# Performance work log

Measured on AMD Instinct MI355X. Metric: run time of the kernel, lower is better.

Reference implementation:

```python
import jax, jax.numpy as jnp
import numpy as np
from jax import lax

B, H, W, C = 8, 64, 64, 256  # H must equal W (einsum contraction requires it)
CQ = C // 4


def conv2d(x, w, b, dilation=1):
    # x: NHWC, w: HWIO (TF Conv2D layout), padding 'same'
    y = lax.conv_general_dilated(
        x, w, window_strides=(1, 1), padding='SAME',
        rhs_dilation=(dilation, dilation),
        dimension_numbers=('NHWC', 'HWIO', 'NHWC'))
    return y + b


def setup_inputs() -> dict:
    key = jax.random.key(0)
    ks = jax.random.split(key, 16)
    s = 0.05
    inp = {
        'x':   jax.random.normal(ks[0], (B, H, W, C), jnp.float32),
        'wq':  jax.random.normal(ks[1], (1, 1, C, CQ), jnp.float32) * s,
        'bq':  jnp.zeros((CQ,), jnp.float32),
        'wq1': jax.random.normal(ks[2], (3, 3, C, CQ), jnp.float32) * s,
        'bq1': jnp.zeros((CQ,), jnp.float32),
        'wq2': jax.random.normal(ks[3], (3, 3, C, CQ), jnp.float32) * s,
        'bq2': jnp.zeros((CQ,), jnp.float32),
        'wq3': jax.random.normal(ks[4], (3, 3, C, CQ), jnp.float32) * s,
        'bq3': jnp.zeros((CQ,), jnp.float32),
        'wq4': jax.random.normal(ks[5], (1, 1, C, C), jnp.float32) * s,
        'bq4': jnp.zeros((C,), jnp.float32),
        'wk':  jax.random.normal(ks[6], (3, 3, C, C), jnp.float32) * s,
        'bk':  jnp.zeros((C,), jnp.float32),
        'wv':  jax.random.normal(ks[7], (1, 1, C, C), jnp.float32) * s,
        'bv':  jnp.zeros((C,), jnp.float32),
        'gamma': jax.random.normal(ks[8], (1,), jnp.float32) * 0.1,
    }
    return inp


def reference(x, wq, bq, wq1, bq1, wq2, bq2, wq3, bq3, wq4, bq4,
              wk, bk, wv, bv, gamma):
    # multi-scale query branch: 1x1, 3x3, 3x3 dil=3, 3x3 dil=6 -> concat -> 1x1
    q = jnp.concatenate([
        conv2d(x, wq, bq, 1),
        conv2d(x, wq1, bq1, 1),
        conv2d(x, wq2, bq2, 3),
        conv2d(x, wq3, bq3, 6),
    ], axis=-1)
    q = conv2d(q, wq4, bq4, 1)                 # (B,H,W,C)
    # key conv applied twice with the SAME weights (as in the original code)
    k = conv2d(conv2d(x, wk, bk, 1), wk, bk, 1)  # (B,H,W,C)
    v = conv2d(x, wv, bv, 1)                    # (B,H,W,C)

    qT = jnp.transpose(q, (0, 2, 1, 3))         # (B,W,H,C)
    # per-channel spatial contraction; requires H == W
    energy = jnp.einsum('bijc,bkjc->bikc', k, qT)   # (B,H,W,C)
    attention = jax.nn.softmax(energy, axis=-1)     # softmax over CHANNEL axis
    attnT = jnp.transpose(attention, (0, 2, 1, 3))  # (B,W,H,C)
    out = jnp.einsum('bijc,bkjc->bikc', attnT, v)   # (B,W,H,C)
    return gamma * out + x
```

## Files before the change

kernel.cpp:

```cpp
#include <hip/hip_runtime.h>

typedef short  short8 __attribute__((ext_vector_type(8)));
typedef short  sv4    __attribute__((ext_vector_type(4)));
typedef __bf16 bf16x8 __attribute__((ext_vector_type(8)));
typedef float  f32x4  __attribute__((ext_vector_type(4)));

__device__ __forceinline__ float bf2f(short s) {
    unsigned u = ((unsigned)(unsigned short)s) << 16;
    return __builtin_bit_cast(float, u);
}
__device__ __forceinline__ short f2bf(float f) {
    unsigned u = __builtin_bit_cast(unsigned, f);
    u += 0x7fffu + ((u >> 16) & 1u);
    return (short)(u >> 16);
}
__device__ __forceinline__ f32x4 mfma16(short8 a, short8 b, f32x4 c) {
    return __builtin_amdgcn_mfma_f32_16x16x32_bf16(
        __builtin_bit_cast(bf16x8, a), __builtin_bit_cast(bf16x8, b), c, 0, 0, 0);
}
__device__ __forceinline__ void gl16(const short* g, short* l) {
    __builtin_amdgcn_global_load_lds(
        (const __attribute__((address_space(1))) void*)g,
        (__attribute__((address_space(3))) void*)l, 16, 0, 0);
}


__global__ __launch_bounds__(256) void detect_k(const short* x, int* flag)
{
    __shared__ int red[256];
    int t = threadIdx.x;
    int cnt = 0;
    for (int i = t; i < 4096; i += 256) {
        int e = (x[2 * i] >> 7) & 0xFF;
        cnt += (e >= 100 && e <= 140) ? 1 : 0;
    }
    red[t] = cnt; __syncthreads();
    for (int s = 128; s > 0; s >>= 1) { if (t < s) red[t] += red[t + s]; __syncthreads(); }
    if (t == 0) *flag = (red[0] < 3277) ? 1 : 0;
}

__global__ __launch_bounds__(256) void convert_x(const void* x, short* xb, const int* flagp)
{
    int f32 = *flagp;
    size_t i = ((size_t)blockIdx.x * 256 + threadIdx.x) * 8;
    short8 v;
    if (f32) {
        const float* fs = (const float*)x + i;
        f32x4 a = *(const f32x4*)fs;
        f32x4 b = *(const f32x4*)(fs + 4);
#pragma unroll
        for (int l = 0; l < 4; l++) { v[l] = f2bf(a[l]); v[4 + l] = f2bf(b[l]); }
    } else {
        v = *(const short8*)((const short*)x + i);
    }
    *(short8*)(xb + i) = v;
}

struct Ptrs {
    const void *wq, *wq1, *wq2, *wq3, *wq4, *wk, *wv;
    const void *bq, *bq1, *bq2, *bq3, *bq4, *bk, *bv, *gm;
};

__global__ __launch_bounds__(256) void convert_k(Ptrs P, short* wp, short* bb, const int* flagp)
{
    int f32 = *flagp;
    int idx = blockIdx.x * 256 + threadIdx.x;
    if (idx < 1179648) {
        const void* src; int Cout, base;
        if      (idx <   16384) { src = P.wq;  Cout =  64; base = 0; }
        else if (idx <  163840) { src = P.wq1; Cout =  64; base = 16384; }
        else if (idx <  311296) { src = P.wq2; Cout =  64; base = 163840; }
        else if (idx <  458752) { src = P.wq3; Cout =  64; base = 311296; }
        else if (idx <  524288) { src = P.wq4; Cout = 256; base = 458752; }
        else if (idx < 1114112) { src = P.wk;  Cout = 256; base = 524288; }
        else                    { src = P.wv;  Cout = 256; base = 1114112; }
        int rem = idx - base;
        int t   = rem / (Cout * 256);
        int r2  = rem - t * Cout * 256;
        int co  = r2 >> 8;
        int ci  = r2 & 255;
        int si  = (t * 256 + ci) * Cout + co;
        wp[idx] = f32 ? f2bf(((const float*)src)[si]) : ((const short*)src)[si];
    } else if (idx < 1179648 + 1280) {
        int j = idx - 1179648;
        if (j < 1025) {
            const void* src; int off;
            if      (j <   64) { src = P.bq;  off = j; }
            else if (j <  128) { src = P.bq1; off = j - 64; }
            else if (j <  192) { src = P.bq2; off = j - 128; }
            else if (j <  256) { src = P.bq3; off = j - 192; }
            else if (j <  512) { src = P.bq4; off = j - 256; }
            else if (j <  768) { src = P.bk;  off = j - 512; }
            else if (j < 1024) { src = P.bv;  off = j - 768; }
            else               { src = P.gm;  off = 0; }
            bb[j] = f32 ? f2bf(((const float*)src)[off]) : ((const short*)src)[off];
        } else if (j >= 1032) {
            bb[j] = 0;
        }
    }
}

struct C8Job {
    const short* src;
    short*       dst;
    const short* wpk;
    const short* bias;
    int outmode;
};

__global__ __launch_bounds__(512, 2) void conv8_tile(C8Job J, const short* zp)
{
    __shared__ short Sh[49152];
    int tid  = threadIdx.x;
    int wid  = tid >> 6, lane = tid & 63;
    int bid  = blockIdx.x;
    int Mtile = (bid & 7) * 32 + (bid >> 3);
    int p0 = Mtile * 128;
    int b  = p0 >> 12;
    int h0 = (p0 >> 6) & 63;

    int lrow = lane & 15, quad = lane >> 4;
    int lr8  = lane >> 3;
    int cl   = (lane & 7) ^ (lr8 & 7);
    int m_base = (wid >> 2) * 64;
    int n_base = (wid & 3) * 64;

    const short* aroot[2]; unsigned vmask[2];
#pragma unroll
    for (int jj = 0; jj < 2; jj++) {
        int m  = (jj * 8 + wid) * 8 + lr8;
        int hh = h0 + (m >> 6);
        int ww = m & 63;
        aroot[jj] = J.src + (((b * 64 + hh) * 64 + ww) * 256 + cl * 8);
        unsigned msk = 0;
#pragma unroll
        for (int t = 0; t < 9; ++t) {
            int dy = t / 3 - 1, dx = t % 3 - 1;
            bool v = ((unsigned)(hh + dy) < 64u) && ((unsigned)(ww + dx) < 64u);
            msk |= (v ? 1u : 0u) << t;
        }
        vmask[jj] = msk;
    }
    const short* wroot[4];
#pragma unroll
    for (int jj = 0; jj < 4; jj++) {
        int n = (jj * 8 + wid) * 8 + lr8;
        wroot[jj] = J.wpk + n * 256 + cl * 8;
    }

    auto STAGE = [&](int step) {
        int t = step >> 2, s4 = step & 3;
        int dy = t / 3 - 1, dx = t % 3 - 1;
        int tdel = (dy * 64 + dx) * 256 + s4 * 64;
        short* bufb = Sh + (step & 1) * 24576;
#pragma unroll
        for (int jj = 0; jj < 2; jj++) {
            const short* p = ((vmask[jj] >> t) & 1u) ? (aroot[jj] + tdel) : (zp + s4 * 64);
            gl16(p, bufb + (jj * 8 + wid) * 512);
        }
#pragma unroll
        for (int jj = 0; jj < 4; jj++)
            gl16(wroot[jj] + t * 65536 + s4 * 64, bufb + 8192 + (jj * 8 + wid) * 512);
    };

    f32x4 acc[4][4] = {};
    STAGE(0);
    for (int s = 0; s < 36; ++s) {
        if (s < 35) {
            STAGE(s + 1);
            asm volatile("s_waitcnt vmcnt(6)" ::: "memory");
        } else {
            asm volatile("s_waitcnt vmcnt(0)" ::: "memory");
        }
        __builtin_amdgcn_sched_barrier(0);
        __builtin_amdgcn_s_barrier();
        __builtin_amdgcn_sched_barrier(0);
        const short* bufb = Sh + (s & 1) * 24576;
#pragma unroll
        for (int j = 0; j < 2; j++) {
            int pc = ((j * 4 + quad) ^ (lrow & 7)) * 8;
            short8 a4[4], b4[4];
#pragma unroll
            for (int mi = 0; mi < 4; mi++)
                a4[mi] = *(const short8*)(bufb + (m_base + mi * 16 + lrow) * 64 + pc);
#pragma unroll
            for (int ni = 0; ni < 4; ni++)
                b4[ni] = *(const short8*)(bufb + 8192 + (n_base + ni * 16 + lrow) * 64 + pc);
            __builtin_amdgcn_s_setprio(1);
#pragma unroll
            for (int mi = 0; mi < 4; mi++)
#pragma unroll
                for (int ni = 0; ni < 4; ni++)
                    acc[mi][ni] = mfma16(a4[mi], b4[ni], acc[mi][ni]);
            __builtin_amdgcn_s_setprio(0);
        }
        __builtin_amdgcn_sched_barrier(0);
        __builtin_amdgcn_s_barrier();
        __builtin_amdgcn_sched_barrier(0);
    }

    int rq = quad * 4;
#pragma unroll
    for (int ni = 0; ni < 4; ni++) {
        int co = n_base + ni * 16 + lrow;
        float bv = bf2f(J.bias[co]);
        if (J.outmode == 0) {
#pragma unroll
            for (int mi = 0; mi < 4; mi++) {
                int pb = p0 + m_base + mi * 16 + rq;
#pragma unroll
                for (int r = 0; r < 4; r++)
                    J.dst[(size_t)(pb + r) * 256 + co] = f2bf(acc[mi][ni][r] + bv);
            }
        } else {
            int hw = h0 + (m_base >> 6);
            short* row = J.dst + ((size_t)(b * 256 + co) * 64 + hw) * 64;
#pragma unroll
            for (int mi = 0; mi < 4; mi++) {
                sv4 o;
#pragma unroll
                for (int r = 0; r < 4; r++) o[r] = f2bf(acc[mi][ni][r] + bv);
                *(sv4*)(row + mi * 16 + rq) = o;
            }
        }
    }
}

struct CJob {
    const short* src;
    short*       dst;
    const short* wpk;
    const short* bias;
    int Cout;
    int dil;
    int ntaps;
    int coff;
    int outmode;
};
struct CTable { CJob j[6]; int end[6]; };

template<int NA, int NB, int BOFS, int WSTEP>
__device__ __forceinline__ void conv_loop(
    const short* src, const short* wpk, int ntaps, int dil,
    const short* zp, short* Sh,
    int wave, int lr8, int cl, int h0, int b, int nt0, int srcT,
    int m_base, int n_base, int lrow, int pc0, int pc1,
    f32x4 (&acc)[4][4])
{
    const short* abase[NA];
    unsigned     vm[NA];
    const short* bbase[NB];
#pragma unroll
    for (int jj = 0; jj < NA; jj++) {
        int m  = (jj * 4 + wave) * 8 + lr8;
        int hh = srcT ? (m & 63) : (h0 + (m >> 6));
        int ww = srcT ? (h0 + (m >> 6)) : (m & 63);
        abase[jj] = src + (((b * 64 + hh) * 64 + ww) * 256 + cl * 8);
        unsigned msk = 1u;
        if (ntaps == 9) {
            msk = 0u;
#pragma unroll
            for (int t = 0; t < 9; ++t) {
                int tr = (t >= 6) ? 2 : ((t >= 3) ? 1 : 0);
                int dy = (tr - 1) * dil, dx = (t - tr * 3 - 1) * dil;
                bool v = ((unsigned)(hh + dy) < 64u) && ((unsigned)(ww + dx) < 64u);
                msk |= (v ? 1u : 0u) << t;
            }
        }
        vm[jj] = msk;
    }
#pragma unroll
    for (int jj = 0; jj < NB; jj++) {
        int n = (jj * 4 + wave) * 8 + lr8;
        bbase[jj] = wpk + (nt0 + n) * 256 + cl * 8;
    }

    int prevdel = 0;
    for (int t = 0; t < ntaps; ++t) {
        int dy = 0, dx = 0;
        if (ntaps == 9) {
            int tr = (t >= 6) ? 2 : ((t >= 3) ? 1 : 0);
            dy = (tr - 1) * dil;
            dx = (t - tr * 3 - 1) * dil;
        }
        int tdel = (dy * 64 + dx) * 256;
        int step = tdel - prevdel; prevdel = tdel;
        const short* pA[NA];
#pragma unroll
        for (int jj = 0; jj < NA; jj++) {
            abase[jj] += step;
            pA[jj] = ((vm[jj] >> t) & 1u) ? abase[jj] : zp;
        }
#pragma unroll
        for (int s4 = 0; s4 < 4; ++s4) {
#pragma unroll
            for (int jj = 0; jj < NA; jj++)
                gl16(pA[jj] + s4 * 64, Sh + (jj * 4 + wave) * 512);
#pragma unroll
            for (int jj = 0; jj < NB; jj++)
                gl16(bbase[jj] + s4 * 64, Sh + BOFS + (jj * 4 + wave) * 512);
            __syncthreads();
#pragma unroll
            for (int j = 0; j < 2; j++) {
                int pc = j ? pc1 : pc0;
                short8 a4[4], b4[4];
#pragma unroll
                for (int mi = 0; mi < 4; mi++)
                    a4[mi] = *(const short8*)(Sh + (m_base + mi * 16 + lrow) * 64 + pc);
#pragma unroll
                for (int ni = 0; ni < 4; ni++)
                    b4[ni] = *(const short8*)(Sh + BOFS + (n_base + ni * 16 + lrow) * 64 + pc);
#pragma unroll
                for (int mi = 0; mi < 4; mi++)
#pragma unroll
                    for (int ni = 0; ni < 4; ni++)
                        acc[mi][ni] = mfma16(a4[mi], b4[ni], acc[mi][ni]);
            }
            __syncthreads();
        }
#pragma unroll
        for (int jj = 0; jj < NB; jj++) bbase[jj] += WSTEP;
    }
}

__global__ __launch_bounds__(256, 3) void conv_tile(CTable T, const short* zp)
{
    __shared__ short Sh[20480];
    int tid = threadIdx.x;
    int bid = blockIdx.x;
    int ji = 0;
    while (ji < 5 && bid >= T.end[ji]) ji++;
    CJob J = T.j[ji];
    int s0  = ji ? T.end[ji - 1] : 0;
    int seg = T.end[ji] - s0;
    int lb  = bid - s0;
    int g   = (lb & 7) * (seg >> 3) + (lb >> 3);

    int big   = (J.Cout == 256);
    int BM    = big ? 128 : 256;
    int ntile = big ? (g & 1) : 0;
    int Mtile = big ? (g >> 1) : g;
    int p0 = Mtile * BM;
    int b  = p0 >> 12;
    int h0 = (p0 >> 6) & 63;
    int nt0  = ntile * 128;
    int srcT = (J.outmode == 3);

    int wave = tid >> 6, lane = tid & 63;
    int lrow = lane & 15, quad = lane >> 4;
    int m_base = big ? (wave & 1) * 64 : wave * 64;
    int n_base = big ? (wave >> 1) * 64 : 0;

    int lr8 = lane >> 3;
    int cl  = (lane & 7) ^ (lr8 & 7);

    int pc0 = ((quad     ^ (lrow & 7)) * 8);
    int pc1 = (((4 + quad) ^ (lrow & 7)) * 8);

    f32x4 acc[4][4] = {};
    if (big)
        conv_loop<4, 4, 8192, 65536>(J.src, J.wpk, J.ntaps, J.dil, zp, Sh,
                                     wave, lr8, cl, h0, b, nt0, srcT,
                                     m_base, n_base, lrow, pc0, pc1, acc);
    else
        conv_loop<8, 2, 16384, 16384>(J.src, J.wpk, J.ntaps, J.dil, zp, Sh,
                                      wave, lr8, cl, h0, b, nt0, srcT,
                                      m_base, n_base, lrow, pc0, pc1, acc);

    int rq = quad * 4;
#pragma unroll
    for (int ni = 0; ni < 4; ni++) {
        int co = nt0 + n_base + ni * 16 + lrow;
        float bv = bf2f(J.bias[co]);
        if (J.outmode == 0) {
#pragma unroll
            for (int mi = 0; mi < 4; mi++) {
                int pb = p0 + m_base + mi * 16 + rq;
#pragma unroll
                for (int r = 0; r < 4; r++)
                    J.dst[(size_t)(pb + r) * 256 + J.coff + co] = f2bf(acc[mi][ni][r] + bv);
            }
        } else {
            int hw = h0 + (m_base >> 6);
            short* row = J.dst + ((size_t)(b * 256 + co) * 64 + hw) * 64;
#pragma unroll
            for (int mi = 0; mi < 4; mi++) {
                sv4 o;
#pragma unroll
                for (int r = 0; r < 4; r++) o[r] = f2bf(acc[mi][ni][r] + bv);
                *(sv4*)(row + mi * 16 + rq) = o;
            }
        }
    }
}

__global__ __launch_bounds__(256) void energy_mfma(const short* qp, const short* kp, float* Et)
{
    int wid  = threadIdx.x >> 6;
    int lane = threadIdx.x & 63;
    int g = blockIdx.x * 4 + wid;
    int b = g >> 8, c = g & 255;
    int lrow = lane & 15;
    int q8   = (lane >> 4) << 3;
    const short* qb = qp + (size_t)(b * 256 + c) * 4096;
    const short* kb = kp + (size_t)(b * 256 + c) * 4096;

    f32x4 acc[4][4] = {};
#pragma unroll
    for (int ks = 0; ks < 2; ++ks) {
        int j0 = ks * 32 + q8;
        short8 A[4], Bv[4];
#pragma unroll
        for (int mi = 0; mi < 4; mi++)
            A[mi] = *(const short8*)(qb + (size_t)(mi * 16 + lrow) * 64 + j0);
#pragma unroll
        for (int ni = 0; ni < 4; ni++)
            Bv[ni] = *(const short8*)(kb + (size_t)(ni * 16 + lrow) * 64 + j0);
#pragma unroll
        for (int mi = 0; mi < 4; mi++)
#pragma unroll
            for (int ni = 0; ni < 4; ni++)
                acc[mi][ni] = mfma16(A[mi], Bv[ni], acc[mi][ni]);
    }
    int rq = (lane >> 4) * 4;
#pragma unroll
    for (int mi = 0; mi < 4; mi++)
#pragma unroll
        for (int r = 0; r < 4; r++) {
            int w = mi * 16 + rq + r;
            float* row = Et + ((size_t)(b * 256 + c) * 64 + w) * 64;
#pragma unroll
            for (int ni = 0; ni < 4; ni++)
                row[ni * 16 + lrow] = acc[mi][ni][r];
        }
}

__global__ __launch_bounds__(256) void softmax_k(const float* Et, short* att)
{
    __shared__ float S[256 * 33];
    __shared__ float red[256];
    __shared__ float sm[256];
    int t  = threadIdx.x;
    int b  = blockIdx.x >> 7;
    int a  = (blockIdx.x >> 1) & 63;
    int jh = blockIdx.x & 1;

    const float* row = Et + ((size_t)(b * 256 + t) * 64 + a) * 64 + jh * 32;
#pragma unroll
    for (int jj = 0; jj < 32; jj += 4) {
        f32x4 v = *(const f32x4*)(row + jj);
#pragma unroll
        for (int l = 0; l < 4; l++) S[t * 33 + jj + l] = v[l];
    }
    __syncthreads();

    int tj = t & 31, tg = t >> 5;
    float m = -1e30f;
#pragma unroll
    for (int cc = 0; cc < 32; ++cc) m = fmaxf(m, S[(tg * 32 + cc) * 33 + tj]);
    red[t] = m;
    __syncthreads();
    if (tg == 0) {
        float mm = red[tj];
#pragma unroll
        for (int gg = 1; gg < 8; ++gg) mm = fmaxf(mm, red[gg * 32 + tj]);
        red[tj] = mm;
    }
    __syncthreads();
    float M = red[tj];
    float s = 0.f;
#pragma unroll
    for (int cc = 0; cc < 32; ++cc) {
        int id = (tg * 32 + cc) * 33 + tj;
        float e = __expf(S[id] - M);
        S[id] = e; s += e;
    }
    sm[t] = s;
    __syncthreads();
    if (tg == 0) {
        float ss = sm[tj];
#pragma unroll
        for (int gg = 1; gg < 8; ++gg) ss += sm[gg * 32 + tj];
        sm[tj] = 1.0f / ss;
    }
    __syncthreads();

    short* orow = att + ((size_t)(b * 256 + t) * 64 + a) * 64 + jh * 32;
#pragma unroll
    for (int jj = 0; jj < 32; jj += 8) {
        short8 o;
#pragma unroll
        for (int l = 0; l < 8; l++) o[l] = f2bf(S[t * 33 + jj + l] * sm[jj + l]);
        *(short8*)(orow + jj) = o;
    }
}

__global__ __launch_bounds__(256) void out_mfma(const short* vp, const short* att, short* G)
{
    int wid  = threadIdx.x >> 6;
    int lane = threadIdx.x & 63;
    int g = blockIdx.x * 4 + wid;
    int b = g >> 8, c = g & 255;
    int lrow = lane & 15;
    int q8   = (lane >> 4) << 3;
    const short* vb = vp  + (size_t)(b * 256 + c) * 4096;
    const short* ab = att + (size_t)(b * 256 + c) * 4096;

    f32x4 acc[4][4] = {};
#pragma unroll
    for (int ks = 0; ks < 2; ++ks) {
        int j0 = ks * 32 + q8;
        short8 A[4], Bv[4];
#pragma unroll
        for (int mi = 0; mi < 4; mi++)
            A[mi] = *(const short8*)(vb + (size_t)(mi * 16 + lrow) * 64 + j0);
#pragma unroll
        for (int ni = 0; ni < 4; ni++)
            Bv[ni] = *(const short8*)(ab + (size_t)(ni * 16 + lrow) * 64 + j0);
#pragma unroll
        for (int mi = 0; mi < 4; mi++)
#pragma unroll
            for (int ni = 0; ni < 4; ni++)
                acc[mi][ni] = mfma16(A[mi], Bv[ni], acc[mi][ni]);
    }
    int rq = (lane >> 4) * 4;
#pragma unroll
    for (int mi = 0; mi < 4; mi++)
#pragma unroll
        for (int r = 0; r < 4; r++) {
            int d = mi * 16 + rq + r;
            short* row = G + ((size_t)(b * 256 + c) * 64 + d) * 64;
#pragma unroll
            for (int ni = 0; ni < 4; ni++)
                row[ni * 16 + lrow] = f2bf(acc[mi][ni][r]);
        }
}

__global__ __launch_bounds__(256) void final_k(const short* G, const void* x,
                                               const void* gamma, void* out, const int* flagp)
{
    int f32 = *flagp;
    int t = threadIdx.x;
    int b = blockIdx.x >> 6, r = blockIdx.x & 63;
    const short* grow = G + ((size_t)(b * 256 + t) * 64 + r) * 64;
    float gm = f32 ? ((const float*)gamma)[0] : bf2f(((const short*)gamma)[0]);
    size_t obase = ((size_t)(b * 64) * 64 + r) * 256 + t;
    if (f32) {
        const float* xs = (const float*)x;
        float* os = (float*)out;
#pragma unroll
        for (int p8 = 0; p8 < 8; p8++) {
            short8 gv = *(const short8*)(grow + p8 * 8);
#pragma unroll
            for (int l = 0; l < 8; l++) {
                size_t off = obase + (size_t)(p8 * 8 + l) * 16384;
                os[off] = gm * bf2f(gv[l]) + xs[off];
            }
        }
    } else {
        const short* xs = (const short*)x;
        short* os = (short*)out;
#pragma unroll
        for (int p8 = 0; p8 < 8; p8++) {
            short8 gv = *(const short8*)(grow + p8 * 8);
#pragma unroll
            for (int l = 0; l < 8; l++) {
                size_t off = obase + (size_t)(p8 * 8 + l) * 16384;
                os[off] = f2bf(gm * bf2f(gv[l]) + bf2f(xs[off]));
            }
        }
    }
}

extern "C" void kernel_launch(void* const* d_in, const int* in_sizes, int n_in,
                              void* d_out, int out_size, void* d_ws, size_t ws_size,
                              hipStream_t stream)
{
    const void* x   = d_in[0];
    Ptrs P{ d_in[1], d_in[3], d_in[5], d_in[7], d_in[9], d_in[11], d_in[13],
            d_in[2], d_in[4], d_in[6], d_in[8], d_in[10], d_in[12], d_in[14], d_in[15] };

    short* ws   = (short*)d_ws;
    short* qcat = ws;
    short* k1   = ws + 8388608;
    short* qp   = ws + 16777216;
    short* kp   = ws + 25165824;
    short* vp   = ws + 33554432;
    short* wp   = ws + 41943040;
    short* bb   = ws + 43122688;
    int*   flag = (int*)(ws + 43123968);
    short* xb   = qp;
    float* Et   = (float*)d_ws;
    short* att  = qp;
    short* G    = kp;
    const short* zp = bb + 1032;

    detect_k<<<1, 256, 0, stream>>>((const short*)x, flag);
    convert_x<<<4096, 256, 0, stream>>>(x, xb, flag);
    convert_k<<<4613, 256, 0, stream>>>(P, wp, bb, flag);

    C8Job A8{ xb, k1, wp + 524288, bb + 512, 0 };
    conv8_tile<<<256, 512, 0, stream>>>(A8, zp);

    CJob j1{ xb, qcat, wp + 16384,   bb + 64,  64,  1, 9, 64,  0 };
    CJob j2{ xb, qcat, wp + 163840,  bb + 128, 64,  3, 9, 128, 0 };
    CJob j3{ xb, qcat, wp + 311296,  bb + 192, 64,  6, 9, 192, 0 };
    CJob jb{ xb, vp,   wp + 1114112, bb + 768, 256, 1, 1, 0,   2 };
    CJob ja{ xb, qcat, wp + 0,       bb + 0,   64,  1, 1, 0,   0 };
    CTable TA{ { j1, j2, j3, jb, ja, ja }, { 128, 256, 384, 896, 1024, 1024 } };
    conv_tile<<<1024, 256, 0, stream>>>(TA, zp);

    C8Job B8{ k1, kp, wp + 524288, bb + 512, 2 };
    conv8_tile<<<256, 512, 0, stream>>>(B8, zp);

    CJob j5{ qcat, qp, wp + 458752, bb + 256, 256, 1, 1, 0, 3 };
    CTable TB{ { j5, j5, j5, j5, j5, j5 }, { 512, 512, 512, 512, 512, 512 } };
    conv_tile<<<512, 256, 0, stream>>>(TB, zp);

    energy_mfma<<<512, 256, 0, stream>>>(qp, kp, Et);
    softmax_k<<<1024, 256, 0, stream>>>(Et, att);
    out_mfma<<<512, 256, 0, stream>>>(vp, att, G);
    final_k<<<512, 256, 0, stream>>>(G, x, d_in[15], d_out, flag);
}
```

Before: 330.1 us.

## Triple-buffer conv8 LDS staging and interleave async loads with MFMA phases

After: 340.8 us. 1.03x slower.

```diff
diff --git a/kernel.cpp b/kernel.cpp
--- a/kernel.cpp
+++ b/kernel.cpp
@@ -110,7 +110,7 @@
 
 __global__ __launch_bounds__(512, 2) void conv8_tile(C8Job J, const short* zp)
 {
-    __shared__ short Sh[49152];
+    __shared__ short Sh[73728];
     int tid  = threadIdx.x;
     int wid  = tid >> 6, lane = tid & 63;
     int bid  = blockIdx.x;
@@ -148,55 +148,93 @@
         wroot[jj] = J.wpk + n * 256 + cl * 8;
     }
 
-    auto STAGE = [&](int step) {
+    auto STAGE_A = [&](int step, short* bufb) {
         int t = step >> 2, s4 = step & 3;
         int dy = t / 3 - 1, dx = t % 3 - 1;
         int tdel = (dy * 64 + dx) * 256 + s4 * 64;
-        short* bufb = Sh + (step & 1) * 24576;
 #pragma unroll
         for (int jj = 0; jj < 2; jj++) {
             const short* p = ((vmask[jj] >> t) & 1u) ? (aroot[jj] + tdel) : (zp + s4 * 64);
             gl16(p, bufb + (jj * 8 + wid) * 512);
         }
-#pragma unroll
-        for (int jj = 0; jj < 4; jj++)
+    };
+    auto STAGE_B = [&](int step, short* bufb, int half) {
+        int t = step >> 2, s4 = step & 3;
+#pragma unroll
+        for (int jj = half * 2; jj < half * 2 + 2; jj++)
             gl16(wroot[jj] + t * 65536 + s4 * 64, bufb + 8192 + (jj * 8 + wid) * 512);
     };
 
+    int pcj0 = ((quad    ) ^ (lrow & 7)) * 8;
+    int pcj1 = ((4 + quad) ^ (lrow & 7)) * 8;
+
     f32x4 acc[4][4] = {};
-    STAGE(0);
+    STAGE_A(0, Sh);          STAGE_B(0, Sh, 0);          STAGE_B(0, Sh, 1);
+    STAGE_A(1, Sh + 24576);  STAGE_B(1, Sh + 24576, 0);  STAGE_B(1, Sh + 24576, 1);
+    asm volatile("s_waitcnt vmcnt(6)" ::: "memory");
+    __builtin_amdgcn_sched_barrier(0);
+    __builtin_amdgcn_s_barrier();
+    __builtin_amdgcn_sched_barrier(0);
+
+    int cur = 0;
     for (int s = 0; s < 36; ++s) {
-        if (s < 35) {
-            STAGE(s + 1);
-            asm volatile("s_waitcnt vmcnt(6)" ::: "memory");
-        } else {
-            asm volatile("s_waitcnt vmcnt(0)" ::: "memory");
-        }
+        int nxt2 = cur + 2; if (nxt2 >= 3) nxt2 -= 3;
+        short* bufc = Sh + cur * 24576;
+        short* bufn = Sh + nxt2 * 24576;
+        bool stg = (s < 34);
+
+        short8 a4[4][2];
+#pragma unroll
+        for (int mi = 0; mi < 4; mi++) {
+            a4[mi][0] = *(const short8*)(bufc + (m_base + mi * 16 + lrow) * 64 + pcj0);
+            a4[mi][1] = *(const short8*)(bufc + (m_base + mi * 16 + lrow) * 64 + pcj1);
+        }
+        {
+            short8 b0 = *(const short8*)(bufc + 8192 + (n_base + lrow) * 64 + pcj0);
+            short8 b1 = *(const short8*)(bufc + 8192 + (n_base + lrow) * 64 + pcj1);
+            if (stg) STAGE_A(s + 2, bufn);
+            __builtin_amdgcn_sched_barrier(0);
+            __builtin_amdgcn_s_barrier();
+            __builtin_amdgcn_sched_barrier(0);
+            __builtin_amdgcn_s_setprio(1);
+#pragma unroll
+            for (int mi = 0; mi < 4; mi++) {
+                acc[mi][0] = mfma16(a4[mi][0], b0, acc[mi][0]);
+                acc[mi][0] = mfma16(a4[mi][1], b1, acc[mi][0]);
+            }
+            __builtin_amdgcn_s_setprio(0);
+            __builtin_amdgcn_sched_barrier(0);
+            __builtin_amdgcn_s_barrier();
+            __builtin_amdgcn_sched_barrier(0);
+        }
+#pragma unroll
+        for (int q = 1; q < 4; ++q) {
+            short8 b0 = *(const short8*)(bufc + 8192 + (n_base + q * 16 + lrow) * 64 + pcj0);
+            short8 b1 = *(const short8*)(bufc + 8192 + (n_base + q * 16 + lrow) * 64 + pcj1);
+            if (q == 1 && stg) STAGE_B(s + 2, bufn, 0);
+            if (q == 2 && stg) STAGE_B(s + 2, bufn, 1);
+            __builtin_amdgcn_sched_barrier(0);
+            __builtin_amdgcn_s_barrier();
+            __builtin_amdgcn_sched_barrier(0);
+            __builtin_amdgcn_s_setprio(1);
+#pragma unroll
+            for (int mi = 0; mi < 4; mi++) {
+                acc[mi][q] = mfma16(a4[mi][0], b0, acc[mi][q]);
+                acc[mi][q] = mfma16(a4[mi][1], b1, acc[mi][q]);
+            }
+            __builtin_amdgcn_s_setprio(0);
+            __builtin_amdgcn_sched_barrier(0);
+            if (q < 3) {
+                __builtin_amdgcn_s_barrier();
+                __builtin_amdgcn_sched_barrier(0);
+            }
+        }
+        if (s <= 33)      { asm volatile("s_waitcnt vmcnt(6)" ::: "memory"); }
+        else if (s == 34) { asm volatile("s_waitcnt vmcnt(0)" ::: "memory"); }
         __builtin_amdgcn_sched_barrier(0);
         __builtin_amdgcn_s_barrier();
         __builtin_amdgcn_sched_barrier(0);
-        const short* bufb = Sh + (s & 1) * 24576;
-#pragma unroll
-        for (int j = 0; j < 2; j++) {
-            int pc = ((j * 4 + quad) ^ (lrow & 7)) * 8;
-            short8 a4[4], b4[4];
-#pragma unroll
-            for (int mi = 0; mi < 4; mi++)
-                a4[mi] = *(const short8*)(bufb + (m_base + mi * 16 + lrow) * 64 + pc);
-#pragma unroll
-            for (int ni = 0; ni < 4; ni++)
-                b4[ni] = *(const short8*)(bufb + 8192 + (n_base + ni * 16 + lrow) * 64 + pc);
-            __builtin_amdgcn_s_setprio(1);
-#pragma unroll
-            for (int mi = 0; mi < 4; mi++)
-#pragma unroll
-                for (int ni = 0; ni < 4; ni++)
-                    acc[mi][ni] = mfma16(a4[mi], b4[ni], acc[mi][ni]);
-            __builtin_amdgcn_s_setprio(0);
-        }
-        __builtin_amdgcn_sched_barrier(0);
-        __builtin_amdgcn_s_barrier();
-        __builtin_amdgcn_sched_barrier(0);
+        cur += 1; if (cur >= 3) cur -= 3;
     }
 
     int rq = quad * 4;
```
